# Performance work log

Measured on AMD Instinct MI355X. Metric: run time of the kernel, lower is better.

The kernel has to match this reference:

```python
import jax, jax.numpy as jnp
import numpy as np

N = 50000   # nodes
E = 800000  # edges
D_IN = 128
DIMS = [(D_IN, 256), (256, 128), (128, 64), (64, 40)]  # per-layer (d_in, d_out)
EPS = 1e-5


def setup_inputs() -> dict:
    key = jax.random.key(0)
    ks = jax.random.split(key, 40)
    inp = {}
    inp["x"] = jax.random.normal(ks[0], (N, D_IN), jnp.float32)
    inp["edge_index"] = jax.random.randint(ks[1], (2, E), 0, N, dtype=jnp.int32)
    ki = 2
    for li, (din, dout) in enumerate(DIMS, 1):
        s = 1.0 / np.sqrt(din)
        inp[f"Wl{li}"] = jax.random.uniform(ks[ki], (din, dout), jnp.float32, -s, s); ki += 1  # SAGE lin_l (neighbor agg), has bias
        inp[f"bl{li}"] = jnp.zeros((dout,), jnp.float32)
        inp[f"Wr{li}"] = jax.random.uniform(ks[ki], (din, dout), jnp.float32, -s, s); ki += 1  # SAGE lin_r (root), no bias
        inp[f"Ws{li}"] = jax.random.uniform(ks[ki], (din, dout), jnp.float32, -s, s); ki += 1  # skip Linear
        inp[f"bs{li}"] = jnp.zeros((dout,), jnp.float32)
        if li < 4:  # BatchNorm only after layers 1-3
            inp[f"g{li}"] = jnp.ones((dout,), jnp.float32)
            inp[f"be{li}"] = jnp.zeros((dout,), jnp.float32)
    return inp


def reference(x, edge_index, Wl1, bl1, Wr1, Ws1, bs1, g1, be1,
              Wl2, bl2, Wr2, Ws2, bs2, g2, be2,
              Wl3, bl3, Wr3, Ws3, bs3, g3, be3,
              Wl4, bl4, Wr4, Ws4, bs4):
    src, dst = edge_index[0], edge_index[1]
    # in-degree counts for mean aggregation (clamped to 1 like PyG)
    cnt = jax.ops.segment_sum(jnp.ones((E,), x.dtype), dst, num_segments=N)
    cnt = jnp.maximum(cnt, 1.0)[:, None]

    def sage(h, Wl, bl, Wr):
        # mean over incoming neighbors, then lin_l(agg) + lin_r(root)
        agg = jax.ops.segment_sum(h[src], dst, num_segments=N) / cnt
        return agg @ Wl + bl + h @ Wr

    def bn(h, g, b):
        mu = h.mean(0)
        var = h.var(0)  # biased variance, as torch BN training mode
        return (h - mu) * jax.lax.rsqrt(var + EPS) * g + b

    h = jax.nn.relu(sage(x, Wl1, bl1, Wr1) + x @ Ws1 + bs1)
    h = bn(h, g1, be1)
    h = jax.nn.relu(sage(h, Wl2, bl2, Wr2) + h @ Ws2 + bs2)
    h = bn(h, g2, be2)
    h = jax.nn.relu(sage(h, Wl3, bl3, Wr3) + h @ Ws3 + bs3)
    h = bn(h, g3, be3)
    return sage(h, Wl4, bl4, Wr4) + h @ Ws4 + bs4
```

## Files before the change

kernel.cpp:

```cpp
#include <hip/hip_runtime.h>


static constexpr int NN = 50000;
static constexpr int NE = 800000;
static constexpr int NP = 50048;

typedef __attribute__((ext_vector_type(8))) short short8;
typedef __attribute__((ext_vector_type(4))) float f32x4;

static constexpr size_t PSTRIDE = (size_t)NP * 32;

__device__ __forceinline__ unsigned short bf16rne(float x) {
  unsigned u = __float_as_uint(x);
  return (unsigned short)((u + 0x7FFFu + ((u >> 16) & 1u)) >> 16);
}
__device__ __forceinline__ float bf2f(unsigned short h) {
  return __uint_as_float(((unsigned)h) << 16);
}

__global__ void count_deg(const int* __restrict__ dst, int* __restrict__ cnt, int E) {
  int e = blockIdx.x * blockDim.x + threadIdx.x;
  if (e < E) atomicAdd(&cnt[dst[e]], 1);
}

__global__ __launch_bounds__(1024) void scan_block(const int* __restrict__ cnt,
                                                   int* __restrict__ excl,
                                                   int* __restrict__ btot, int n) {
  __shared__ int lds[1024];
  int i = blockIdx.x * 1024 + threadIdx.x;
  int v = (i < n) ? cnt[i] : 0;
  lds[threadIdx.x] = v;
  __syncthreads();
#pragma unroll
  for (int off = 1; off < 1024; off <<= 1) {
    int t = 0;
    if ((int)threadIdx.x >= off) t = lds[threadIdx.x - off];
    __syncthreads();
    lds[threadIdx.x] += t;
    __syncthreads();
  }
  if (i < n) excl[i] = lds[threadIdx.x] - v;
  if (threadIdx.x == 1023) btot[blockIdx.x] = lds[1023];
}

__global__ void scan_tops(int* __restrict__ btot, int nb) {
  int t = threadIdx.x;
  int v = (t < nb) ? btot[t] : 0;
  int own = v;
#pragma unroll
  for (int off = 1; off < 64; off <<= 1) {
    int u = __shfl_up(v, off);
    if (t >= off) v += u;
  }
  if (t < nb) btot[t] = v - own;
}

__global__ void finalize_csr(int* __restrict__ offs, const int* __restrict__ btot,
                             const int* __restrict__ cnt, int* __restrict__ cursor,
                             float* __restrict__ inv, int n) {
  int i = blockIdx.x * blockDim.x + threadIdx.x;
  if (i < n) {
    int o = offs[i] + btot[i >> 10];
    offs[i] = o;
    cursor[i] = o;
    int c = cnt[i];
    inv[i] = 1.0f / (float)(c > 0 ? c : 1);
  }
}

__global__ void fill_adj(const int* __restrict__ src, const int* __restrict__ dst,
                         int* __restrict__ cursor, int* __restrict__ adj, int E) {
  int e = blockIdx.x * blockDim.x + threadIdx.x;
  if (e < E) {
    int p = atomicAdd(&cursor[dst[e]], 1);
    adj[p] = src[e];
  }
}

__global__ void pack_x(const float* __restrict__ x, ushort* __restrict__ xP,
                       ushort* __restrict__ xb, int N) {
  int gid = blockIdx.x * 256 + threadIdx.x;
  int row = gid >> 4, kb = gid & 15;
  if (row >= NP) return;
  float v[8];
  if (row < N) {
    float4 a = *(const float4*)&x[(size_t)row * 128 + kb * 8];
    float4 b = *(const float4*)&x[(size_t)row * 128 + kb * 8 + 4];
    v[0]=a.x; v[1]=a.y; v[2]=a.z; v[3]=a.w; v[4]=b.x; v[5]=b.y; v[6]=b.z; v[7]=b.w;
  } else {
#pragma unroll
    for (int j = 0; j < 8; ++j) v[j] = 0.f;
  }
  short8 H, L;
#pragma unroll
  for (int j = 0; j < 8; ++j) {
    unsigned short h = bf16rne(v[j]);
    H[j] = (short)h;
    L[j] = (short)bf16rne(v[j] - bf2f(h));
  }
  *(short8*)&xP[((size_t)(kb * 2) * NP + row) * 8] = H;
  *(short8*)&xP[((size_t)(kb * 2 + 1) * NP + row) * 8] = L;
  *(short8*)&xb[(size_t)(kb >> 2) * PSTRIDE + (size_t)row * 32 + (kb & 3) * 8] = H;
}

template <int L1V>
__global__ void prep_w(const float* __restrict__ Wl, const float* __restrict__ Wr,
                       const float* __restrict__ Wsk, const float* __restrict__ ab,
                       ushort* __restrict__ Wp, int K, int K1, int M, int Mp, int Mpad) {
  int gid = blockIdx.x * 256 + threadIdx.x;
  int col = gid % Mpad, kb = gid / Mpad;
  if (kb >= (K >> 3)) return;
  short8 H, L;
#pragma unroll
  for (int j = 0; j < 8; ++j) {
    int k = kb * 8 + j;
    float v = 0.f;
    if (col < Mp) {
      if (L1V) {
        v = (k < K1) ? Wl[(size_t)k * M + col]
                     : Wr[(size_t)(k - K1) * M + col] + Wsk[(size_t)(k - K1) * M + col];
      } else {
        float w = (col < M) ? Wl[(size_t)k * M + col]
                            : Wr[(size_t)k * M + (col - M)] + Wsk[(size_t)k * M + (col - M)];
        v = ab[k] * w;
      }
    }
    unsigned short h = bf16rne(v);
    H[j] = (short)h;
    L[j] = (short)bf16rne(v - bf2f(h));
  }
  *(short8*)&Wp[((size_t)(kb * 2) * Mpad + col) * 8] = H;
  *(short8*)&Wp[((size_t)(kb * 2 + 1) * Mpad + col) * 8] = L;
}

__global__ void prep_bias(const float* __restrict__ Wl, const float* __restrict__ Wr,
                          const float* __restrict__ Wsk, const float* __restrict__ bl,
                          const float* __restrict__ bs, const float* __restrict__ ab,
                          float* __restrict__ bias2, int K, int M) {
  int c = blockIdx.x;
  int k = threadIdx.x;
  float va = 0.f, vd = 0.f;
  if (k < K) {
    float b = ab[K + k];
    vd = b * Wl[(size_t)k * M + c];
    va = b * (Wr[(size_t)k * M + c] + Wsk[(size_t)k * M + c]);
  }
  __shared__ float r[512];
  r[k] = va;
  r[256 + k] = vd;
  __syncthreads();
  for (int off = 128; off > 0; off >>= 1) {
    if (k < off) {
      r[k] += r[k + off];
      r[256 + k] += r[256 + k + off];
    }
    __syncthreads();
  }
  if (k == 0) {
    bias2[c] = bl[c] + bs[c] + r[0];
    bias2[M + c] = r[256];
  }
}

__global__ __launch_bounds__(256) void aggregate1p(
    const ushort* __restrict__ xb, const int* __restrict__ adj,
    const int* __restrict__ offs, const int* __restrict__ cnt,
    const float* __restrict__ inv, ushort* __restrict__ aggP,
    float* __restrict__ sums, int N) {
  const int tid = threadIdx.x;
  if (blockIdx.x == 0) {
    for (int j = tid; j < 512; j += 256) sums[j] = 0.f;
  }
  const int xcd = blockIdx.x & 7;
  const int p = xcd & 3;
  const int setIdx = (blockIdx.x >> 3) * 2 + (xcd >> 2);
  const int nSets = (gridDim.x >> 3) * 2;
  const int sub = tid >> 3;
  const int c4 = (tid & 7) * 4;
  const int col = p * 32 + c4;
  const ushort* __restrict__ tab = xb + (size_t)p * PSTRIDE + c4;
  const int kb = col >> 3, sl = col & 7;

  for (int n = setIdx * 32 + sub; n < NP; n += nSets * 32) {
    float s0 = 0.f, s1 = 0.f, s2 = 0.f, s3 = 0.f, invn = 0.f;
    if (n < N) {
      invn = inv[n];
      int off = offs[n], deg = cnt[n];
      int i = 0;
      for (; i + 4 <= deg; i += 4) {
        int a0 = adj[off + i + 0];
        int a1 = adj[off + i + 1];
        int a2 = adj[off + i + 2];
        int a3 = adj[off + i + 3];
        ushort4 v0 = *(const ushort4*)&tab[(size_t)a0 * 32];
        ushort4 v1 = *(const ushort4*)&tab[(size_t)a1 * 32];
        ushort4 v2 = *(const ushort4*)&tab[(size_t)a2 * 32];
        ushort4 v3 = *(const ushort4*)&tab[(size_t)a3 * 32];
        s0 += (bf2f(v0.x) + bf2f(v1.x)) + (bf2f(v2.x) + bf2f(v3.x));
        s1 += (bf2f(v0.y) + bf2f(v1.y)) + (bf2f(v2.y) + bf2f(v3.y));
        s2 += (bf2f(v0.z) + bf2f(v1.z)) + (bf2f(v2.z) + bf2f(v3.z));
        s3 += (bf2f(v0.w) + bf2f(v1.w)) + (bf2f(v2.w) + bf2f(v3.w));
      }
      for (; i < deg; ++i) {
        ushort4 v = *(const ushort4*)&tab[(size_t)adj[off + i] * 32];
        s0 += bf2f(v.x); s1 += bf2f(v.y); s2 += bf2f(v.z); s3 += bf2f(v.w);
      }
    }
    float m0 = s0 * invn, m1 = s1 * invn, m2 = s2 * invn, m3 = s3 * invn;
    ushort4 H, L;
    H.x = bf16rne(m0); L.x = bf16rne(m0 - bf2f(H.x));
    H.y = bf16rne(m1); L.y = bf16rne(m1 - bf2f(H.y));
    H.z = bf16rne(m2); L.z = bf16rne(m2 - bf2f(H.z));
    H.w = bf16rne(m3); L.w = bf16rne(m3 - bf2f(H.w));
    size_t chunk = ((size_t)(kb * 2) * NP + n) * 8 + sl;
    *(ushort4*)&aggP[chunk] = H;
    *(ushort4*)&aggP[chunk + (size_t)NP * 8] = L;
  }
}

template <int TWO_A, int EPI, int NK32, int KT1>
__global__ __launch_bounds__(256) void gemm_pk(
    const ushort* __restrict__ A1, const ushort* __restrict__ A2,
    const ushort* __restrict__ B, const float* __restrict__ bl,
    const float* __restrict__ bs, ushort* __restrict__ OutL,
    float* __restrict__ OutR, ushort* __restrict__ OutP,
    float* __restrict__ sums, int N, int M, int Mp, int Mpad) {
  const int tid = threadIdx.x;
  const int l = tid & 63;
  const int w = tid >> 6;
  const int wr = w >> 1, wc = w & 1;
  const int l16 = l & 15, lh = l >> 4;
  const int row0 = blockIdx.x * 128, col0 = blockIdx.y * 128;

  const f32x4 z4 = {0.f, 0.f, 0.f, 0.f};
  f32x4 acc[4][4];
#pragma unroll
  for (int m = 0; m < 4; ++m)
#pragma unroll
    for (int n = 0; n < 4; ++n) acc[m][n] = z4;

  const int arow = row0 + wr * 64 + l16;
  const int bcol = col0 + wc * 64 + l16;

#pragma unroll 2
  for (int it = 0; it < NK32; ++it) {
    const int kbase = it * 32;
    const ushort* Ap = A1;
    int kloc = kbase;
    if (TWO_A && kbase >= KT1) { Ap = A2; kloc = kbase - KT1; }
    const int akb = (kloc >> 3) + lh;
    const int bkb = (kbase >> 3) + lh;
    const ushort* a_hi = Ap + ((size_t)(akb * 2) * NP + arow) * 8;
    const ushort* a_lo = a_hi + (size_t)NP * 8;
    const ushort* b_hi = B + ((size_t)(bkb * 2) * Mpad + bcol) * 8;
    const ushort* b_lo = b_hi + (size_t)Mpad * 8;

    short8 ah[4], al[4], bh[4], blo[4];
#pragma unroll
    for (int m = 0; m < 4; ++m) {
      ah[m] = *(const short8*)(a_hi + m * 128);
      al[m] = *(const short8*)(a_lo + m * 128);
    }
#pragma unroll
    for (int n = 0; n < 4; ++n) {
      bh[n] = *(const short8*)(b_hi + n * 128);
      blo[n] = *(const short8*)(b_lo + n * 128);
    }
#pragma unroll
    for (int m = 0; m < 4; ++m)
#pragma unroll
      for (int n = 0; n < 4; ++n) {
        acc[m][n] = __builtin_amdgcn_mfma_f32_16x16x32_bf16(ah[m], bh[n], acc[m][n], 0, 0, 0);
        acc[m][n] = __builtin_amdgcn_mfma_f32_16x16x32_bf16(ah[m], blo[n], acc[m][n], 0, 0, 0);
        acc[m][n] = __builtin_amdgcn_mfma_f32_16x16x32_bf16(al[m], bh[n], acc[m][n], 0, 0, 0);
      }
  }

  const int lr = lh * 4;
  if (EPI) {
    __shared__ float st[2048];
    float cs[4] = {0.f, 0.f, 0.f, 0.f}, cq[4] = {0.f, 0.f, 0.f, 0.f};
#pragma unroll
    for (int n = 0; n < 4; ++n) {
      int col = col0 + wc * 64 + n * 16 + l16;
      bool cok = col < Mp;
      float bias = cok ? (bl[col] + bs[col]) : 0.f;
      int cb = col >> 3, ch = col & 7;
      size_t hbase = ((size_t)(cb * 2) * NP) * 8 + ch;
      size_t lbase = hbase + (size_t)NP * 8;
#pragma unroll
      for (int m = 0; m < 4; ++m)
#pragma unroll
        for (int i = 0; i < 4; ++i) {
          int row = row0 + wr * 64 + m * 16 + lr + i;
          float v = acc[m][n][i] + bias;
          v = fmaxf(v, 0.f);
          if (cok && row < N) {
            unsigned short hh = bf16rne(v);
            OutP[hbase + (size_t)row * 8] = hh;
            OutP[lbase + (size_t)row * 8] = bf16rne(v - bf2f(hh));
            cs[n] += v;
            cq[n] += v * v;
          }
        }
    }
    int slot = wr * 4 + lh;
#pragma unroll
    for (int n = 0; n < 4; ++n) {
      int c = wc * 64 + n * 16 + l16;
      st[c * 8 + slot] = cs[n];
      st[1024 + c * 8 + slot] = cq[n];
    }
    __syncthreads();
    if (tid < 128) {
      float s1 = 0.f, s2 = 0.f;
#pragma unroll
      for (int t2 = 0; t2 < 8; ++t2) {
        s1 += st[tid * 8 + t2];
        s2 += st[1024 + tid * 8 + t2];
      }
      int c = col0 + tid;
      if (c < Mp) {
        atomicAdd(&sums[c], s1);
        atomicAdd(&sums[Mp + c], s2);
      }
    }
  } else {
#pragma unroll
    for (int n = 0; n < 4; ++n) {
      int col = col0 + wc * 64 + n * 16 + l16;
      if (col >= Mp) continue;
      bool isL = col < M;
      int colR = col - M;
      size_t lblk = (size_t)(col >> 5) * PSTRIDE + (col & 31);
#pragma unroll
      for (int m = 0; m < 4; ++m)
#pragma unroll
        for (int i = 0; i < 4; ++i) {
          int row = row0 + wr * 64 + m * 16 + lr + i;
          if (row < N) {
            float v = acc[m][n][i];
            if (isL) OutL[lblk + (size_t)row * 32] = bf16rne(v);
            else     OutR[(size_t)row * M + colR] = v;
          }
        }
    }
  }
}

template <int NPLOG, int M, int RELU, int STATS, int PACK>
__global__ __launch_bounds__(256) void combineP(
    const ushort* __restrict__ Zl, const float* __restrict__ Zr,
    const int* __restrict__ adj, const int* __restrict__ offs,
    const int* __restrict__ cnt, const float* __restrict__ inv,
    const float* __restrict__ bias2, float* __restrict__ outF,
    ushort* __restrict__ outP, float* __restrict__ sums, int N) {
  constexpr int NPASS = 1 << NPLOG;
  constexpr int XCDG = 8 >> NPLOG;
  const int tid = threadIdx.x;
  const int xcd = blockIdx.x & 7;
  const int p = xcd & (NPASS - 1);
  const int setIdx = (blockIdx.x >> 3) * XCDG + (xcd >> NPLOG);
  const int nSets = (gridDim.x >> 3) * XCDG;
  const int sub = tid >> 3;
  const int c4 = (tid & 7) * 4;
  const int col = p * 32 + c4;
  const bool act = col < M;

  float ba0 = 0, ba1 = 0, ba2 = 0, ba3 = 0, bd0 = 0, bd1 = 0, bd2 = 0, bd3 = 0;
  if (act) {
    float4 ba = *(const float4*)&bias2[col];
    float4 bd = *(const float4*)&bias2[M + col];
    ba0 = ba.x; ba1 = ba.y; ba2 = ba.z; ba3 = ba.w;
    bd0 = bd.x; bd1 = bd.y; bd2 = bd.z; bd3 = bd.w;
  }
  float cs[4] = {0.f, 0.f, 0.f, 0.f}, cq[4] = {0.f, 0.f, 0.f, 0.f};
  const ushort* __restrict__ tab = Zl + (size_t)p * PSTRIDE + c4;
  const int kb = col >> 3, sl = col & 7;

  for (int n = setIdx * 32 + sub; n < N; n += nSets * 32) {
    if (act) {
      int off = offs[n], deg = cnt[n];
      float s0 = 0.f, s1 = 0.f, s2 = 0.f, s3 = 0.f;
      int i = 0;
      for (; i + 4 <= deg; i += 4) {
        int a0 = adj[off + i + 0];
        int a1 = adj[off + i + 1];
        int a2 = adj[off + i + 2];
        int a3 = adj[off + i + 3];
        ushort4 v0 = *(const ushort4*)&tab[(size_t)a0 * 32];
        ushort4 v1 = *(const ushort4*)&tab[(size_t)a1 * 32];
        ushort4 v2 = *(const ushort4*)&tab[(size_t)a2 * 32];
        ushort4 v3 = *(const ushort4*)&tab[(size_t)a3 * 32];
        s0 += (bf2f(v0.x) + bf2f(v1.x)) + (bf2f(v2.x) + bf2f(v3.x));
        s1 += (bf2f(v0.y) + bf2f(v1.y)) + (bf2f(v2.y) + bf2f(v3.y));
        s2 += (bf2f(v0.z) + bf2f(v1.z)) + (bf2f(v2.z) + bf2f(v3.z));
        s3 += (bf2f(v0.w) + bf2f(v1.w)) + (bf2f(v2.w) + bf2f(v3.w));
      }
      for (; i < deg; ++i) {
        ushort4 v = *(const ushort4*)&tab[(size_t)adj[off + i] * 32];
        s0 += bf2f(v.x); s1 += bf2f(v.y); s2 += bf2f(v.z); s3 += bf2f(v.w);
      }
      float invn = inv[n];
      float4 zr = *(const float4*)&Zr[(size_t)n * M + col];
      float y0 = fmaf(s0, invn, zr.x + ba0);
      float y1 = fmaf(s1, invn, zr.y + ba1);
      float y2 = fmaf(s2, invn, zr.z + ba2);
      float y3 = fmaf(s3, invn, zr.w + ba3);
      if (deg > 0) { y0 += bd0; y1 += bd1; y2 += bd2; y3 += bd3; }
      if (RELU) {
        y0 = fmaxf(y0, 0.f); y1 = fmaxf(y1, 0.f);
        y2 = fmaxf(y2, 0.f); y3 = fmaxf(y3, 0.f);
      }
      if (PACK) {
        ushort4 H, L;
        H.x = bf16rne(y0); L.x = bf16rne(y0 - bf2f(H.x));
        H.y = bf16rne(y1); L.y = bf16rne(y1 - bf2f(H.y));
        H.z = bf16rne(y2); L.z = bf16rne(y2 - bf2f(H.z));
        H.w = bf16rne(y3); L.w = bf16rne(y3 - bf2f(H.w));
        size_t chunk = ((size_t)(kb * 2) * NP + n) * 8 + sl;
        *(ushort4*)&outP[chunk] = H;
        *(ushort4*)&outP[chunk + (size_t)NP * 8] = L;
      } else {
        *(float4*)&outF[(size_t)n * M + col] = make_float4(y0, y1, y2, y3);
      }
      if (STATS) {
        cs[0] += y0; cs[1] += y1; cs[2] += y2; cs[3] += y3;
        cq[0] += y0 * y0; cq[1] += y1 * y1; cq[2] += y2 * y2; cq[3] += y3 * y3;
      }
    }
  }
  if (STATS) {
    __shared__ float st1[32 * 32], st2[32 * 32];
#pragma unroll
    for (int j = 0; j < 4; ++j) {
      st1[sub * 32 + c4 + j] = cs[j];
      st2[sub * 32 + c4 + j] = cq[j];
    }
    __syncthreads();
    if (tid < 32) {
      float s1 = 0.f, s2 = 0.f;
#pragma unroll
      for (int t2 = 0; t2 < 32; ++t2) {
        s1 += st1[t2 * 32 + tid];
        s2 += st2[t2 * 32 + tid];
      }
      int c = p * 32 + tid;
      if (c < M) {
        atomicAdd(&sums[c], s1);
        atomicAdd(&sums[M + c], s2);
      }
    }
  }
}

__global__ void bn_affine(float* __restrict__ sums, const float* __restrict__ g,
                          const float* __restrict__ be, float* __restrict__ ab,
                          int M, float invN) {
  int j = threadIdx.x;
  if (j < M) {
    float s1 = sums[j], s2 = sums[M + j];
    float mu = s1 * invN;
    float var = fmaf(-mu, mu, s2 * invN);
    float a = g[j] / sqrtf(var + 1e-5f);
    ab[j] = a;
    ab[M + j] = fmaf(-mu, a, be[j]);
    sums[j] = 0.f;
    sums[M + j] = 0.f;
  }
}

extern "C" void kernel_launch(void* const* d_in, const int* in_sizes, int n_in,
                              void* d_out, int out_size, void* d_ws, size_t ws_size,
                              hipStream_t stream) {
  const int N = NN, E = NE;
  const float* x = (const float*)d_in[0];
  const int* ei = (const int*)d_in[1];
  const int* srcs = ei;
  const int* dsts = ei + E;

  const float* Wl1 = (const float*)d_in[2];
  const float* bl1 = (const float*)d_in[3];
  const float* Wr1 = (const float*)d_in[4];
  const float* Ws1 = (const float*)d_in[5];
  const float* bs1 = (const float*)d_in[6];
  const float* g1  = (const float*)d_in[7];
  const float* be1 = (const float*)d_in[8];
  const float* Wl2 = (const float*)d_in[9];
  const float* bl2 = (const float*)d_in[10];
  const float* Wr2 = (const float*)d_in[11];
  const float* Ws2 = (const float*)d_in[12];
  const float* bs2 = (const float*)d_in[13];
  const float* g2  = (const float*)d_in[14];
  const float* be2 = (const float*)d_in[15];
  const float* Wl3 = (const float*)d_in[16];
  const float* bl3 = (const float*)d_in[17];
  const float* Wr3 = (const float*)d_in[18];
  const float* Ws3 = (const float*)d_in[19];
  const float* bs3 = (const float*)d_in[20];
  const float* g3  = (const float*)d_in[21];
  const float* be3 = (const float*)d_in[22];
  const float* Wl4 = (const float*)d_in[23];
  const float* bl4 = (const float*)d_in[24];
  const float* Wr4 = (const float*)d_in[25];
  const float* Ws4 = (const float*)d_in[26];
  const float* bs4 = (const float*)d_in[27];

  char* wsB = (char*)d_ws;
  ushort* hAP = (ushort*)wsB;
  ushort* hCP = hAP;
  ushort* xP  = (ushort*)(wsB + 51249152);
  ushort* hBP = xP;
  char* regC  = wsB + 51249152 + 25624576;
  ushort* aggP = (ushort*)regC;
  float* Zr   = (float*)regC;
  char* regD  = regC + 25624576;
  ushort* xb  = (ushort*)regD;
  ushort* Zl  = (ushort*)regD;
  char* p = regD + (size_t)NP * 128 * 2;
  ushort* W1p = (ushort*)p; p += 262144;
  ushort* W2p = (ushort*)p; p += 262144;
  ushort* W3p = (ushort*)p; p += 65536;
  ushort* W4p = (ushort*)p; p += 32768;
  float* sums = (float*)p; p += 512 * 4;
  float* ab   = (float*)p; p += 512 * 4;
  float* bias2 = (float*)p; p += 256 * 4;
  float* invc = (float*)p; p += (size_t)N * 4;
  int* cnt    = (int*)p; p += (size_t)N * 4;
  int* offs   = (int*)p; p += (size_t)N * 4;
  int* cursor = (int*)p; p += (size_t)N * 4;
  int* btot   = (int*)p; p += 256;
  int* adj    = (int*)p;

  hipMemsetAsync(cnt, 0, sizeof(int) * N, stream);
  int eb = (E + 255) / 256;
  int nb = (N + 1023) / 1024;
  count_deg<<<eb, 256, 0, stream>>>(dsts, cnt, E);
  scan_block<<<nb, 1024, 0, stream>>>(cnt, offs, btot, N);
  scan_tops<<<1, 64, 0, stream>>>(btot, nb);
  finalize_csr<<<(N + 255) / 256, 256, 0, stream>>>(offs, btot, cnt, cursor, invc, N);
  fill_adj<<<eb, 256, 0, stream>>>(srcs, dsts, cursor, adj, E);

  pack_x<<<NP * 16 / 256, 256, 0, stream>>>(x, xP, xb, N);
  prep_w<1><<<32 * 256 / 256, 256, 0, stream>>>(Wl1, Wr1, Ws1, nullptr, W1p,
                                                256, 128, 256, 256, 256);

  const int RB = NP / 128;
  const int GP = 4096;
  const float invN = 1.0f / (float)N;

  aggregate1p<<<GP, 256, 0, stream>>>(xb, adj, offs, cnt, invc, aggP, sums, N);
  gemm_pk<1, 1, 8, 128><<<dim3(RB, 2), 256, 0, stream>>>(
      aggP, xP, W1p, bl1, bs1, nullptr, nullptr, hAP, sums, N, 256, 256, 256);
  bn_affine<<<1, 256, 0, stream>>>(sums, g1, be1, ab, 256, invN);

  prep_w<0><<<32 * 256 / 256, 256, 0, stream>>>(Wl2, Wr2, Ws2, ab, W2p,
                                                256, 0, 128, 256, 256);
  prep_bias<<<128, 256, 0, stream>>>(Wl2, Wr2, Ws2, bl2, bs2, ab, bias2, 256, 128);
  gemm_pk<0, 0, 8, 0><<<dim3(RB, 2), 256, 0, stream>>>(
      hAP, nullptr, W2p, nullptr, nullptr, Zl, Zr, nullptr, nullptr, N, 128, 256, 256);
  combineP<2, 128, 1, 1, 1><<<GP, 256, 0, stream>>>(
      Zl, Zr, adj, offs, cnt, invc, bias2, nullptr, hBP, sums, N);
  bn_affine<<<1, 128, 0, stream>>>(sums, g2, be2, ab, 128, invN);

  prep_w<0><<<16 * 128 / 256, 256, 0, stream>>>(Wl3, Wr3, Ws3, ab, W3p,
                                                128, 0, 64, 128, 128);
  prep_bias<<<64, 256, 0, stream>>>(Wl3, Wr3, Ws3, bl3, bs3, ab, bias2, 128, 64);
  gemm_pk<0, 0, 4, 0><<<dim3(RB, 1), 256, 0, stream>>>(
      hBP, nullptr, W3p, nullptr, nullptr, Zl, Zr, nullptr, nullptr, N, 64, 128, 128);
  combineP<1, 64, 1, 1, 1><<<GP, 256, 0, stream>>>(
      Zl, Zr, adj, offs, cnt, invc, bias2, nullptr, hCP, sums, N);
  bn_affine<<<1, 64, 0, stream>>>(sums, g3, be3, ab, 64, invN);

  prep_w<0><<<8 * 128 / 256, 256, 0, stream>>>(Wl4, Wr4, Ws4, ab, W4p,
                                               64, 0, 40, 80, 128);
  prep_bias<<<40, 256, 0, stream>>>(Wl4, Wr4, Ws4, bl4, bs4, ab, bias2, 64, 40);
  gemm_pk<0, 0, 2, 0><<<dim3(RB, 1), 256, 0, stream>>>(
      hCP, nullptr, W4p, nullptr, nullptr, Zl, Zr, nullptr, nullptr, N, 40, 80, 128);
  combineP<1, 40, 0, 0, 0><<<GP, 256, 0, stream>>>(
      Zl, Zr, adj, offs, cnt, invc, bias2, (float*)d_out, nullptr, nullptr, N);
}
```

Baseline: 539.3 us.

## Pad CSR rows to multiples of eight and gather neighbor indices via shuffles

Each node's adjacency segment is padded to a multiple of eight and filled with a dummy index that points at a zero row (the padding rows of the packed tables, now written as zeros). This lets the gather loop run without a remainder loop. Each 8-lane group loads eight indices with one coalesced load and broadcasts them with shuffles, instead of every lane loading every index. The cost is an extra kernel to fill the dummy entries, a larger adjacency array, and wasted gathers on padding entries, which can be up to seven per node.

Result: faster. 527.2 us (-2.2%).

```diff
diff --git a/kernel.cpp b/kernel.cpp
--- a/kernel.cpp
+++ b/kernel.cpp
@@ -4,6 +4,7 @@
 static constexpr int NN = 50000;
 static constexpr int NE = 800000;
 static constexpr int NP = 50048;
+static constexpr int NADJ = NE + 7 * NN;
 
 typedef __attribute__((ext_vector_type(8))) short short8;
 typedef __attribute__((ext_vector_type(4))) float f32x4;
@@ -28,7 +29,7 @@
                                                    int* __restrict__ btot, int n) {
   __shared__ int lds[1024];
   int i = blockIdx.x * 1024 + threadIdx.x;
-  int v = (i < n) ? cnt[i] : 0;
+  int v = (i < n) ? ((cnt[i] + 7) & ~7) : 0;
   lds[threadIdx.x] = v;
   __syncthreads();
 #pragma unroll
@@ -66,6 +67,11 @@
     int c = cnt[i];
     inv[i] = 1.0f / (float)(c > 0 ? c : 1);
   }
+}
+
+__global__ void fill_dummy(int* __restrict__ adj, int n) {
+  int i = blockIdx.x * blockDim.x + threadIdx.x;
+  if (i < n) adj[i] = NN;
 }
 
 __global__ void fill_adj(const int* __restrict__ src, const int* __restrict__ dst,
@@ -162,6 +168,31 @@
   }
 }
 
+#define GATHER8(tab, base)                                                    \
+  {                                                                           \
+    int aj = adj[base + k8];                                                  \
+    int a0 = __shfl(aj, gb + 0), a1 = __shfl(aj, gb + 1);                     \
+    int a2 = __shfl(aj, gb + 2), a3 = __shfl(aj, gb + 3);                     \
+    int a4 = __shfl(aj, gb + 4), a5 = __shfl(aj, gb + 5);                     \
+    int a6 = __shfl(aj, gb + 6), a7 = __shfl(aj, gb + 7);                     \
+    ushort4 v0 = *(const ushort4*)&tab[(size_t)a0 * 32];                      \
+    ushort4 v1 = *(const ushort4*)&tab[(size_t)a1 * 32];                      \
+    ushort4 v2 = *(const ushort4*)&tab[(size_t)a2 * 32];                      \
+    ushort4 v3 = *(const ushort4*)&tab[(size_t)a3 * 32];                      \
+    ushort4 v4 = *(const ushort4*)&tab[(size_t)a4 * 32];                      \
+    ushort4 v5 = *(const ushort4*)&tab[(size_t)a5 * 32];                      \
+    ushort4 v6 = *(const ushort4*)&tab[(size_t)a6 * 32];                      \
+    ushort4 v7 = *(const ushort4*)&tab[(size_t)a7 * 32];                      \
+    s0 += ((bf2f(v0.x) + bf2f(v1.x)) + (bf2f(v2.x) + bf2f(v3.x))) +          \
+          ((bf2f(v4.x) + bf2f(v5.x)) + (bf2f(v6.x) + bf2f(v7.x)));           \
+    s1 += ((bf2f(v0.y) + bf2f(v1.y)) + (bf2f(v2.y) + bf2f(v3.y))) +          \
+          ((bf2f(v4.y) + bf2f(v5.y)) + (bf2f(v6.y) + bf2f(v7.y)));           \
+    s2 += ((bf2f(v0.z) + bf2f(v1.z)) + (bf2f(v2.z) + bf2f(v3.z))) +          \
+          ((bf2f(v4.z) + bf2f(v5.z)) + (bf2f(v6.z) + bf2f(v7.z)));           \
+    s3 += ((bf2f(v0.w) + bf2f(v1.w)) + (bf2f(v2.w) + bf2f(v3.w))) +          \
+          ((bf2f(v4.w) + bf2f(v5.w)) + (bf2f(v6.w) + bf2f(v7.w)));           \
+  }
+
 __global__ __launch_bounds__(256) void aggregate1p(
     const ushort* __restrict__ xb, const int* __restrict__ adj,
     const int* __restrict__ offs, const int* __restrict__ cnt,
@@ -175,6 +206,9 @@
   const int p = xcd & 3;
   const int setIdx = (blockIdx.x >> 3) * 2 + (xcd >> 2);
   const int nSets = (gridDim.x >> 3) * 2;
+  const int lane = tid & 63;
+  const int gb = lane & 56;
+  const int k8 = lane & 7;
   const int sub = tid >> 3;
   const int c4 = (tid & 7) * 4;
   const int col = p * 32 + c4;
@@ -185,26 +219,9 @@
     float s0 = 0.f, s1 = 0.f, s2 = 0.f, s3 = 0.f, invn = 0.f;
     if (n < N) {
       invn = inv[n];
-      int off = offs[n], deg = cnt[n];
-      int i = 0;
-      for (; i + 4 <= deg; i += 4) {
-        int a0 = adj[off + i + 0];
-        int a1 = adj[off + i + 1];
-        int a2 = adj[off + i + 2];
-        int a3 = adj[off + i + 3];
-        ushort4 v0 = *(const ushort4*)&tab[(size_t)a0 * 32];
-        ushort4 v1 = *(const ushort4*)&tab[(size_t)a1 * 32];
-        ushort4 v2 = *(const ushort4*)&tab[(size_t)a2 * 32];
-        ushort4 v3 = *(const ushort4*)&tab[(size_t)a3 * 32];
-        s0 += (bf2f(v0.x) + bf2f(v1.x)) + (bf2f(v2.x) + bf2f(v3.x));
-        s1 += (bf2f(v0.y) + bf2f(v1.y)) + (bf2f(v2.y) + bf2f(v3.y));
-        s2 += (bf2f(v0.z) + bf2f(v1.z)) + (bf2f(v2.z) + bf2f(v3.z));
-        s3 += (bf2f(v0.w) + bf2f(v1.w)) + (bf2f(v2.w) + bf2f(v3.w));
-      }
-      for (; i < deg; ++i) {
-        ushort4 v = *(const ushort4*)&tab[(size_t)adj[off + i] * 32];
-        s0 += bf2f(v.x); s1 += bf2f(v.y); s2 += bf2f(v.z); s3 += bf2f(v.w);
-      }
+      int off = offs[n];
+      int pdeg = (cnt[n] + 7) & ~7;
+      for (int i = 0; i < pdeg; i += 8) GATHER8(tab, off + i);
     }
     float m0 = s0 * invn, m1 = s1 * invn, m2 = s2 * invn, m3 = s3 * invn;
     ushort4 H, L;
@@ -338,10 +355,11 @@
 #pragma unroll
         for (int i = 0; i < 4; ++i) {
           int row = row0 + wr * 64 + m * 16 + lr + i;
-          if (row < N) {
-            float v = acc[m][n][i];
-            if (isL) OutL[lblk + (size_t)row * 32] = bf16rne(v);
-            else     OutR[(size_t)row * M + colR] = v;
+          float v = acc[m][n][i];
+          if (isL) {
+            OutL[lblk + (size_t)row * 32] = (row < N) ? bf16rne(v) : (ushort)0;
+          } else if (row < N) {
+            OutR[(size_t)row * M + colR] = v;
           }
         }
     }
@@ -362,6 +380,9 @@
   const int p = xcd & (NPASS - 1);
   const int setIdx = (blockIdx.x >> 3) * XCDG + (xcd >> NPLOG);
   const int nSets = (gridDim.x >> 3) * XCDG;
+  const int lane = tid & 63;
+  const int gb = lane & 56;
+  const int k8 = lane & 7;
   const int sub = tid >> 3;
   const int c4 = (tid & 7) * 4;
   const int col = p * 32 + c4;
@@ -379,28 +400,11 @@
   const int kb = col >> 3, sl = col & 7;
 
   for (int n = setIdx * 32 + sub; n < N; n += nSets * 32) {
+    int off = offs[n], deg = cnt[n];
+    int pdeg = (deg + 7) & ~7;
+    float s0 = 0.f, s1 = 0.f, s2 = 0.f, s3 = 0.f;
+    for (int i = 0; i < pdeg; i += 8) GATHER8(tab, off + i);
     if (act) {
-      int off = offs[n], deg = cnt[n];
-      float s0 = 0.f, s1 = 0.f, s2 = 0.f, s3 = 0.f;
-      int i = 0;
-      for (; i + 4 <= deg; i += 4) {
-        int a0 = adj[off + i + 0];
-        int a1 = adj[off + i + 1];
-        int a2 = adj[off + i + 2];
-        int a3 = adj[off + i + 3];
-        ushort4 v0 = *(const ushort4*)&tab[(size_t)a0 * 32];
-        ushort4 v1 = *(const ushort4*)&tab[(size_t)a1 * 32];
-        ushort4 v2 = *(const ushort4*)&tab[(size_t)a2 * 32];
-        ushort4 v3 = *(const ushort4*)&tab[(size_t)a3 * 32];
-        s0 += (bf2f(v0.x) + bf2f(v1.x)) + (bf2f(v2.x) + bf2f(v3.x));
-        s1 += (bf2f(v0.y) + bf2f(v1.y)) + (bf2f(v2.y) + bf2f(v3.y));
-        s2 += (bf2f(v0.z) + bf2f(v1.z)) + (bf2f(v2.z) + bf2f(v3.z));
-        s3 += (bf2f(v0.w) + bf2f(v1.w)) + (bf2f(v2.w) + bf2f(v3.w));
-      }
-      for (; i < deg; ++i) {
-        ushort4 v = *(const ushort4*)&tab[(size_t)adj[off + i] * 32];
-        s0 += bf2f(v.x); s1 += bf2f(v.y); s2 += bf2f(v.z); s3 += bf2f(v.w);
-      }
       float invn = inv[n];
       float4 zr = *(const float4*)&Zr[(size_t)n * M + col];
       float y0 = fmaf(s0, invn, zr.x + ba0);
@@ -539,6 +543,7 @@
   scan_block<<<nb, 1024, 0, stream>>>(cnt, offs, btot, N);
   scan_tops<<<1, 64, 0, stream>>>(btot, nb);
   finalize_csr<<<(N + 255) / 256, 256, 0, stream>>>(offs, btot, cnt, cursor, invc, N);
+  fill_dummy<<<(NADJ + 255) / 256, 256, 0, stream>>>(adj, NADJ);
   fill_adj<<<eb, 256, 0, stream>>>(srcs, dsts, cursor, adj, E);
 
   pack_x<<<NP * 16 / 256, 256, 0, stream>>>(x, xP, xb, N);
```
